# Performance work log

Measured on AMD Instinct MI355X. Metric: run time of the kernel, lower is better.

Reference implementation:

```python
import jax, jax.numpy as jnp
import numpy as np

EPS = 1e-8


def setup_inputs() -> dict:
    key = jax.random.key(0)
    ks = jax.random.split(key, 6)
    B, Cin, Cout, K, S, G = 8, 64, 64, 3, 512, 48
    fan_in = Cin * K * K * K
    bound_w = np.sqrt(6.0 / ((1 + 0.25 ** 2) * fan_in))  # kaiming_uniform a=0.25
    bound_b = 1.0 / np.sqrt(fan_in)
    bound_lin = 1.0 / np.sqrt(S)
    return {
        "x": jax.random.normal(ks[0], (B, Cin, G, G, G), jnp.float32),
        "style": jax.random.normal(ks[1], (B, S), jnp.float32),
        "weight": jax.random.uniform(ks[2], (Cout, Cin, K, K, K), jnp.float32, -bound_w, bound_w),
        "bias": jax.random.uniform(ks[3], (1, Cout, 1, 1, 1), jnp.float32, -bound_b, bound_b),
        "style_w": jax.random.uniform(ks[4], (Cin, S), jnp.float32, -bound_lin, bound_lin),
        "style_b": jax.random.uniform(ks[5], (Cin,), jnp.float32, -bound_lin, bound_lin),
    }


def reference(x, style, weight, bias, style_w, style_b):
    B, Cin = x.shape[0], x.shape[1]
    Cout, K = weight.shape[0], weight.shape[2]
    # style modulation scale per (sample, input channel)
    s = style @ style_w.T + style_b                      # [B, Cin]
    # modulate: per-sample weights [B, Cout, Cin, K, K, K]
    w = weight[None] * s[:, None, :, None, None, None]
    # demodulate: rsqrt of per-(sample, out-channel) variance
    var = jnp.sum(w * w, axis=(2, 3, 4, 5), keepdims=True)
    w = w * jax.lax.rsqrt(var + EPS)
    # grouped conv: merge batch into channels, groups = batch_size
    w = w.reshape(B * Cout, Cin, K, K, K)
    xg = x.reshape(1, B * Cin, *x.shape[2:])
    y = jax.lax.conv_general_dilated(
        xg, w,
        window_strides=(1, 1, 1),
        padding='VALID',
        dimension_numbers=('NCDHW', 'OIDHW', 'NCDHW'),
        feature_group_count=B,
    )
    y = y.reshape(B, Cout, *y.shape[2:])
    return y + bias
```

## Files before the change

### kernel.cpp

```cpp
#include <hip/hip_runtime.h>


typedef __bf16 bf16x8 __attribute__((ext_vector_type(8)));
typedef float  f32x4  __attribute__((ext_vector_type(4)));

static constexpr int   B_   = 8;
static constexpr int   S_   = 512;
static constexpr int   G_   = 48;
static constexpr int   O_   = 46;
static constexpr int   TAPS = 27;
static constexpr int   SPI  = G_ * G_ * G_;
static constexpr int   SPO  = O_ * O_ * O_;
static constexpr float EPSV = 1e-8f;

static constexpr size_t XT_OFF   = 0;
static constexpr size_t XT_BYTES = (size_t)B_ * SPI * 64 * 2;
static constexpr size_t WQ_OFF   = XT_OFF + XT_BYTES;

__device__ __forceinline__ unsigned short f2bf(float f) {
    unsigned int u = __float_as_uint(f);
    u = (u + 0x7fffu + ((u >> 16) & 1u)) >> 16;
    return (unsigned short)u;
}

__global__ __launch_bounds__(256) void prep_kernel(
    const float* __restrict__ style,
    const float* __restrict__ style_w,
    const float* __restrict__ style_b,
    const float* __restrict__ weight,
    unsigned short* __restrict__ wq)
{
    __shared__ float s_sh[64];
    __shared__ float d_sh[64];
    const int b = blockIdx.x, t = threadIdx.x;

    {
        const int g = t >> 2, q = t & 3;
        const float4* sp = (const float4*)(style + b * S_) + q * 32;
        const float4* wp = (const float4*)(style_w + g * S_) + q * 32;
        float acc = 0.f;
#pragma unroll
        for (int i = 0; i < 32; ++i) {
            const float4 a = sp[i], w4 = wp[i];
            acc += a.x * w4.x + a.y * w4.y + a.z * w4.z + a.w * w4.w;
        }
        acc += __shfl_xor(acc, 1);
        acc += __shfl_xor(acc, 2);
        if (q == 0) s_sh[g] = acc + style_b[g];
    }
    __syncthreads();

    {
        const int co = t >> 2, q = t & 3;
        float v = 0.f;
#pragma unroll 1
        for (int j = 0; j < 16; ++j) {
            const int ci = q * 16 + j;
            const float sv = s_sh[ci];
            const float* wp = weight + (co * 64 + ci) * TAPS;
#pragma unroll
            for (int i = 0; i < TAPS; ++i) { const float x = wp[i] * sv; v += x * x; }
        }
        v += __shfl_xor(v, 1);
        v += __shfl_xor(v, 2);
        if (q == 0) d_sh[co] = rsqrtf(v + EPSV);
    }
    __syncthreads();

#pragma unroll 1
    for (int it = 0; it < 2; ++it) {
        const int item = t + it * 256;
        const int kc = item >> 8;
        const int g  = (item >> 6) & 3;
        const int l  = item & 63;
        const int co = g * 16 + (l & 15);
        const int ci0 = kc * 32 + ((l >> 4) * 8);
        const float dd = d_sh[co];
#pragma unroll 1
        for (int tap = 0; tap < TAPS; ++tap) {
            unsigned int u[4];
#pragma unroll
            for (int k = 0; k < 4; ++k) {
                const int ci = ci0 + 2 * k;
                const float w0 = weight[(co * 64 + ci)     * TAPS + tap] * s_sh[ci]     * dd;
                const float w1 = weight[(co * 64 + ci + 1) * TAPS + tap] * s_sh[ci + 1] * dd;
                u[k] = (unsigned)f2bf(w0) | ((unsigned)f2bf(w1) << 16);
            }
            uint4 v; v.x = u[0]; v.y = u[1]; v.z = u[2]; v.w = u[3];
            *(uint4*)(wq + ((size_t)((b * 2 + kc) * 27 + tap)) * 2048 + (g * 64 + l) * 8) = v;
        }
    }
}

__global__ void xT_kernel(const float* __restrict__ x,
                          unsigned short* __restrict__ xT)
{
    const int blk = blockIdx.x;
    const int b = blk / 1728;
    const int sp0 = (blk - b * 1728) * 64;
    const int t = threadIdx.x;
    __shared__ float tile[64][65];

    const int cr = t >> 4;
    const int s4 = (t & 15) * 4;
#pragma unroll
    for (int r = 0; r < 4; ++r) {
        const int ci = r * 16 + cr;
        const float4 v = *(const float4*)(x + ((size_t)b * 64 + ci) * SPI + sp0 + s4);
        tile[ci][s4]     = v.x;
        tile[ci][s4 + 1] = v.y;
        tile[ci][s4 + 2] = v.z;
        tile[ci][s4 + 3] = v.w;
    }
    __syncthreads();

    const int ci8 = (t & 7) * 8;
    const int spq = t >> 3;
#pragma unroll
    for (int p = 0; p < 2; ++p) {
        const int sp = spq + 32 * p;
        unsigned int u[4];
#pragma unroll
        for (int k = 0; k < 4; ++k) {
            const unsigned int lo = f2bf(tile[ci8 + 2 * k][sp]);
            const unsigned int hi = f2bf(tile[ci8 + 2 * k + 1][sp]);
            u[k] = lo | (hi << 16);
        }
        uint4 v; v.x = u[0]; v.y = u[1]; v.z = u[2]; v.w = u[3];
        *(uint4*)(xT + ((size_t)b * SPI + sp0 + sp) * 64 + ci8) = v;
    }
}

#define XST     80
#define XTILE_B (648 * 80)

#define MFMA16(AS, BS)                                                        \
    do {                                                                      \
        __builtin_amdgcn_s_setprio(1);                                        \
        _Pragma("unroll")                                                     \
        for (int g_ = 0; g_ < 4; ++g_) {                                      \
            _Pragma("unroll")                                                 \
            for (int n_ = 0; n_ < 4; ++n_)                                    \
                acc[g_ * 4 + n_] = __builtin_amdgcn_mfma_f32_16x16x32_bf16(   \
                    AS[g_], BS[n_], acc[g_ * 4 + n_], 0, 0, 0);               \
        }                                                                     \
        __builtin_amdgcn_s_setprio(0);                                        \
    } while (0)

__global__ __launch_bounds__(256, 3) void conv_kernel(
    const unsigned short* __restrict__ xT,
    const unsigned short* __restrict__ wq,
    const float* __restrict__ bias,
    float* __restrict__ out)
{
    __shared__ __align__(16) char xs[XTILE_B];

    const int t = threadIdx.x;
    const int p  = blockIdx.x;
    const int lg = (p & 7) * 432 + (p >> 3);
    const int xt = lg % 3;
    const int r0 = lg / 3;
    const int yt = r0 % 12;
    const int bz = r0 / 12;
    const int b  = bz / 12, zt = bz - b * 12;
    const int x0 = xt * 16;
    const int y0 = (yt < 11) ? yt * 4 : 42;
    const int z0 = (zt < 11) ? zt * 4 : 42;

    const unsigned short* const xb = xT + (size_t)b * (SPI * 64);
    const unsigned short* const wb = wq + (size_t)b * (2 * TAPS * 2048);

    const int w = t >> 6, l = t & 63, kg = l >> 4, l16 = l & 15;
    const unsigned short* const wa = wb + l * 8;
    const int bbase = (w * 108 + l16) * XST + kg * 16;

    f32x4 acc[16];
#pragma unroll
    for (int i = 0; i < 16; ++i) acc[i] = (f32x4){0.f, 0.f, 0.f, 0.f};

    bf16x8 aA[4], aB[4], bA[4], bB[4];

    auto x_src = [&](int i, int kc) -> const uint4* {
        const int sp = i >> 2, cg = i & 3;
        const int iz = sp / 108;
        const int r1 = sp - iz * 108;
        const int iy = r1 / 18;
        const int ix = r1 - iy * 18;
        int gx = x0 + ix; if (gx > 47) gx = 47;
        return (const uint4*)(xb +
            ((((z0 + iz) * 48) + (y0 + iy)) * 48 + gx) * 64 + kc * 32 + cg * 8);
    };

#pragma unroll 1
    for (int kc = 0; kc < 2; ++kc) {
        const int base = kc * TAPS;

#pragma unroll
        for (int g = 0; g < 4; ++g) {
            aA[g] = *(const bf16x8*)(wa + (size_t)(base    ) * 2048 + g * 512);
            aB[g] = *(const bf16x8*)(wa + (size_t)(base + 1) * 2048 + g * 512);
        }

        if (kc) __syncthreads();

#pragma unroll
        for (int j = 0; j < 10; ++j) {
            const int i = t + j * 256;
            const uint4 v = *x_src(i, kc);
            *(uint4*)(xs + (i >> 2) * XST + (i & 3) * 16) = v;
        }
        if (t < 32) {
            const int i = 2560 + t;
            const uint4 v = *x_src(i, kc);
            *(uint4*)(xs + (i >> 2) * XST + (i & 3) * 16) = v;
        }
        __syncthreads();

#pragma unroll
        for (int nf = 0; nf < 4; ++nf)
            bA[nf] = *(const bf16x8*)(xs + bbase + nf * (18 * XST));

#pragma unroll 1
        for (int j = 0; j < 13; ++j) {
            const int t0 = 2 * j;
            {
                const int tb = t0 + 1;
                const int kz = tb / 9, rr = tb - kz * 9;
                const int ky = rr / 3, kx = rr - ky * 3;
                const int toff = (kz * 108 + ky * 18 + kx) * XST;
#pragma unroll
                for (int nf = 0; nf < 4; ++nf)
                    bB[nf] = *(const bf16x8*)(xs + toff + bbase + nf * (18 * XST));
                MFMA16(aA, bA);
                const size_t ao = (size_t)(base + t0 + 2) * 2048;
#pragma unroll
                for (int g = 0; g < 4; ++g)
                    aA[g] = *(const bf16x8*)(wa + ao + g * 512);
            }
            {
                const int tb = t0 + 2;
                const int kz = tb / 9, rr = tb - kz * 9;
                const int ky = rr / 3, kx = rr - ky * 3;
                const int toff = (kz * 108 + ky * 18 + kx) * XST;
#pragma unroll
                for (int nf = 0; nf < 4; ++nf)
                    bA[nf] = *(const bf16x8*)(xs + toff + bbase + nf * (18 * XST));
                MFMA16(aB, bB);
                int ta = base + t0 + 3; if (ta > 53) ta = 53;
                const size_t ao = (size_t)ta * 2048;
#pragma unroll
                for (int g = 0; g < 4; ++g)
                    aB[g] = *(const bf16x8*)(wa + ao + g * 512);
            }
        }
        MFMA16(aA, bA);
    }

    const size_t ob = (size_t)b * 64 * SPO;
    const int oz = z0 + w;
    const int ox = x0 + l16;
    if (ox < O_) {
#pragma unroll
        for (int g = 0; g < 4; ++g) {
#pragma unroll
            for (int nt = 0; nt < 4; ++nt) {
                const int oy = y0 + nt;
                const f32x4 v = acc[g * 4 + nt];
                const size_t so = (size_t)oz * 2116 + oy * 46 + ox;
#pragma unroll
                for (int r = 0; r < 4; ++r) {
                    const int co = g * 16 + kg * 4 + r;
                    out[ob + (size_t)co * SPO + so] = v[r] + bias[co];
                }
            }
        }
    }
}

extern "C" void kernel_launch(void* const* d_in, const int* in_sizes, int n_in,
                              void* d_out, int out_size, void* d_ws, size_t ws_size,
                              hipStream_t stream)
{
    const float* x       = (const float*)d_in[0];
    const float* style   = (const float*)d_in[1];
    const float* weight  = (const float*)d_in[2];
    const float* bias    = (const float*)d_in[3];
    const float* style_w = (const float*)d_in[4];
    const float* style_b = (const float*)d_in[5];
    float* out = (float*)d_out;

    char* ws = (char*)d_ws;
    unsigned short* xT  = (unsigned short*)(ws + XT_OFF);
    unsigned short* wqp = (unsigned short*)(ws + WQ_OFF);

    hipLaunchKernelGGL(prep_kernel, dim3(B_), dim3(256), 0, stream,
                       style, style_w, style_b, weight, wqp);
    hipLaunchKernelGGL(xT_kernel, dim3(B_ * (SPI / 64)), dim3(256), 0, stream,
                       x, xT);
    hipLaunchKernelGGL(conv_kernel, dim3(3456), dim3(256), 0, stream,
                       xT, wqp, bias, out);
}
```

Measured before the change: 619.4 us.

## Split weight prep into parallel kernels and load conv input tile via global_load_lds

The single 8-block prep kernel is replaced by three kernels for style projection, demodulation factors and bf16 weight packing, each launched over many more blocks so the prep stage stops being serialized on a few CUs. In the conv kernel the input tile staging now uses direct global-to-LDS loads instead of going through registers, and the LDS row stride drops from 80 to 64 to match that contiguous layout. The unpadded stride may add LDS bank conflicts on the B-fragment reads, and the extra launches add some overhead.

```diff
diff --git a/kernel.cpp b/kernel.cpp
--- a/kernel.cpp
+++ b/kernel.cpp
@@ -16,6 +16,12 @@
 static constexpr size_t XT_OFF   = 0;
 static constexpr size_t XT_BYTES = (size_t)B_ * SPI * 64 * 2;
 static constexpr size_t WQ_OFF   = XT_OFF + XT_BYTES;
+static constexpr size_t WQ_BYTES = (size_t)B_ * 2 * TAPS * 64 * 32 * 2;
+static constexpr size_t S_OFF    = WQ_OFF + WQ_BYTES;
+static constexpr size_t D_OFF    = S_OFF + 2048;
+
+typedef const void __attribute__((address_space(1)))* gas_cvp;
+typedef void __attribute__((address_space(3)))*       las_vp;
 
 __device__ __forceinline__ unsigned short f2bf(float f) {
     unsigned int u = __float_as_uint(f);
@@ -23,51 +29,47 @@
     return (unsigned short)u;
 }
 
-__global__ __launch_bounds__(256) void prep_kernel(
-    const float* __restrict__ style,
-    const float* __restrict__ style_w,
-    const float* __restrict__ style_b,
-    const float* __restrict__ weight,
-    unsigned short* __restrict__ wq)
-{
-    __shared__ float s_sh[64];
-    __shared__ float d_sh[64];
-    const int b = blockIdx.x, t = threadIdx.x;
-
-    {
-        const int g = t >> 2, q = t & 3;
-        const float4* sp = (const float4*)(style + b * S_) + q * 32;
-        const float4* wp = (const float4*)(style_w + g * S_) + q * 32;
-        float acc = 0.f;
-#pragma unroll
-        for (int i = 0; i < 32; ++i) {
-            const float4 a = sp[i], w4 = wp[i];
-            acc += a.x * w4.x + a.y * w4.y + a.z * w4.z + a.w * w4.w;
-        }
-        acc += __shfl_xor(acc, 1);
-        acc += __shfl_xor(acc, 2);
-        if (q == 0) s_sh[g] = acc + style_b[g];
-    }
-    __syncthreads();
-
-    {
-        const int co = t >> 2, q = t & 3;
-        float v = 0.f;
-#pragma unroll 1
-        for (int j = 0; j < 16; ++j) {
-            const int ci = q * 16 + j;
-            const float sv = s_sh[ci];
-            const float* wp = weight + (co * 64 + ci) * TAPS;
-#pragma unroll
-            for (int i = 0; i < TAPS; ++i) { const float x = wp[i] * sv; v += x * x; }
-        }
-        v += __shfl_xor(v, 1);
-        v += __shfl_xor(v, 2);
-        if (q == 0) d_sh[co] = rsqrtf(v + EPSV);
-    }
-    __syncthreads();
-
-#pragma unroll 1
+__global__ void s_kernel(const float* __restrict__ style,
+                         const float* __restrict__ style_w,
+                         const float* __restrict__ style_b,
+                         float* __restrict__ s_out)
+{
+    const int bg = blockIdx.x, b = bg >> 6, g = bg & 63, l = threadIdx.x;
+    const float4* sp = (const float4*)(style + b * S_);
+    const float4* wp = (const float4*)(style_w + g * S_);
+    const float4 a0 = sp[l * 2], a1 = sp[l * 2 + 1];
+    const float4 b0 = wp[l * 2], b1 = wp[l * 2 + 1];
+    float acc = a0.x * b0.x + a0.y * b0.y + a0.z * b0.z + a0.w * b0.w
+              + a1.x * b1.x + a1.y * b1.y + a1.z * b1.z + a1.w * b1.w;
+#pragma unroll
+    for (int m = 1; m <= 32; m <<= 1) acc += __shfl_xor(acc, m);
+    if (l == 0) s_out[bg] = acc + style_b[g];
+}
+
+__global__ void d_kernel(const float* __restrict__ weight,
+                         const float* __restrict__ s,
+                         float* __restrict__ d_out)
+{
+    const int bc = blockIdx.x, b = bc >> 6, co = bc & 63, ci = threadIdx.x;
+    const float sv = s[b * 64 + ci];
+    const float* wp = weight + (co * 64 + ci) * TAPS;
+    float v = 0.f;
+#pragma unroll
+    for (int i = 0; i < TAPS; ++i) { const float t = wp[i] * sv; v += t * t; }
+#pragma unroll
+    for (int m = 1; m <= 32; m <<= 1) v += __shfl_xor(v, m);
+    if (ci == 0) d_out[bc] = rsqrtf(v + EPSV);
+}
+
+__global__ void wq_kernel(const float* __restrict__ weight,
+                          const float* __restrict__ s,
+                          const float* __restrict__ d,
+                          unsigned short* __restrict__ wq)
+{
+    const int blk = blockIdx.x;
+    const int b = blk / 27, tap = blk - b * 27;
+    const int t = threadIdx.x;
+#pragma unroll
     for (int it = 0; it < 2; ++it) {
         const int item = t + it * 256;
         const int kc = item >> 8;
@@ -75,20 +77,17 @@
         const int l  = item & 63;
         const int co = g * 16 + (l & 15);
         const int ci0 = kc * 32 + ((l >> 4) * 8);
-        const float dd = d_sh[co];
-#pragma unroll 1
-        for (int tap = 0; tap < TAPS; ++tap) {
-            unsigned int u[4];
-#pragma unroll
-            for (int k = 0; k < 4; ++k) {
-                const int ci = ci0 + 2 * k;
-                const float w0 = weight[(co * 64 + ci)     * TAPS + tap] * s_sh[ci]     * dd;
-                const float w1 = weight[(co * 64 + ci + 1) * TAPS + tap] * s_sh[ci + 1] * dd;
-                u[k] = (unsigned)f2bf(w0) | ((unsigned)f2bf(w1) << 16);
-            }
-            uint4 v; v.x = u[0]; v.y = u[1]; v.z = u[2]; v.w = u[3];
-            *(uint4*)(wq + ((size_t)((b * 2 + kc) * 27 + tap)) * 2048 + (g * 64 + l) * 8) = v;
-        }
+        const float dd = d[b * 64 + co];
+        unsigned int u[4];
+#pragma unroll
+        for (int k = 0; k < 4; ++k) {
+            const int ci = ci0 + 2 * k;
+            const float w0 = weight[(co * 64 + ci)     * TAPS + tap] * s[b * 64 + ci]     * dd;
+            const float w1 = weight[(co * 64 + ci + 1) * TAPS + tap] * s[b * 64 + ci + 1] * dd;
+            u[k] = (unsigned)f2bf(w0) | ((unsigned)f2bf(w1) << 16);
+        }
+        uint4 v; v.x = u[0]; v.y = u[1]; v.z = u[2]; v.w = u[3];
+        *(uint4*)(wq + ((size_t)((b * 2 + kc) * 27 + tap)) * 2048 + (g * 64 + l) * 8) = v;
     }
 }
 
@@ -131,8 +130,8 @@
     }
 }
 
-#define XST     80
-#define XTILE_B (648 * 80)
+#define XST     64
+#define XTILE_B (648 * 64)
 
 #define MFMA16(AS, BS)                                                        \
     do {                                                                      \
@@ -206,13 +205,13 @@
 #pragma unroll
         for (int j = 0; j < 10; ++j) {
             const int i = t + j * 256;
-            const uint4 v = *x_src(i, kc);
-            *(uint4*)(xs + (i >> 2) * XST + (i & 3) * 16) = v;
+            __builtin_amdgcn_global_load_lds((gas_cvp)x_src(i, kc),
+                                             (las_vp)(xs + i * 16), 16, 0, 0);
         }
         if (t < 32) {
             const int i = 2560 + t;
             const uint4 v = *x_src(i, kc);
-            *(uint4*)(xs + (i >> 2) * XST + (i & 3) * 16) = v;
+            *(uint4*)(xs + i * 16) = v;
         }
         __syncthreads();
 
@@ -292,9 +291,15 @@
     char* ws = (char*)d_ws;
     unsigned short* xT  = (unsigned short*)(ws + XT_OFF);
     unsigned short* wqp = (unsigned short*)(ws + WQ_OFF);
-
-    hipLaunchKernelGGL(prep_kernel, dim3(B_), dim3(256), 0, stream,
-                       style, style_w, style_b, weight, wqp);
+    float* sbuf = (float*)(ws + S_OFF);
+    float* dbuf = (float*)(ws + D_OFF);
+
+    hipLaunchKernelGGL(s_kernel, dim3(512), dim3(64), 0, stream,
+                       style, style_w, style_b, sbuf);
+    hipLaunchKernelGGL(d_kernel, dim3(512), dim3(64), 0, stream,
+                       weight, sbuf, dbuf);
+    hipLaunchKernelGGL(wq_kernel, dim3(216), dim3(256), 0, stream,
+                       weight, sbuf, dbuf, wqp);
     hipLaunchKernelGGL(xT_kernel, dim3(B_ * (SPI / 64)), dim3(256), 0, stream,
                        x, xT);
     hipLaunchKernelGGL(conv_kernel, dim3(3456), dim3(256), 0, stream,
```

After: 555.4 us. -10.3%, faster.
